# Kernel tuning notes

Hardware: AMD Instinct MI355X
Metric: run time of the kernel (lower is better)

Reference implementation:

```python
import jax, jax.numpy as jnp
import numpy as np

N_NODES = 50000
N_EDGES = 800000
D = 128
H = 128


def setup_inputs() -> dict:
    key = jax.random.key(0)
    ks = jax.random.split(key, 8)
    s = 1.0 / np.sqrt(D)
    return {
        "x": jax.random.normal(ks[0], (N_NODES, D), dtype=jnp.float32),
        "edge_index": jax.random.randint(ks[1], (2, N_EDGES), 0, N_NODES, dtype=jnp.int64),
        "W1_l": jax.random.normal(ks[2], (D, H), dtype=jnp.float32) * s,
        "b1_l": jax.random.normal(ks[3], (H,), dtype=jnp.float32) * s,
        "W1_r": jax.random.normal(ks[4], (D, H), dtype=jnp.float32) * s,
        "W2_l": jax.random.normal(ks[5], (H, H), dtype=jnp.float32) * s,
        "b2_l": jax.random.normal(ks[6], (H,), dtype=jnp.float32) * s,
        "W2_r": jax.random.normal(ks[7], (H, H), dtype=jnp.float32) * s,
    }


def _sage_conv(x, src, dst, W_l, b_l, W_r, n_nodes):
    # mean aggregation of source features at destination nodes
    agg = jax.ops.segment_sum(x[src], dst, num_segments=n_nodes)          # [N, d]
    cnt = jax.ops.segment_sum(jnp.ones((src.shape[0],), x.dtype), dst,
                              num_segments=n_nodes)                        # [N]
    mean = agg / jnp.maximum(cnt, 1.0)[:, None]
    out = mean @ W_l + b_l + x @ W_r                                       # [N, h]
    # L2 normalize (normalize=True in SAGEConv)
    norm = jnp.linalg.norm(out, axis=-1, keepdims=True)
    return out / jnp.maximum(norm, 1e-12)


def reference(x, edge_index, W1_l, b1_l, W1_r, W2_l, b2_l, W2_r):
    src, dst = edge_index[0], edge_index[1]
    n = x.shape[0]
    h = jax.nn.relu(_sage_conv(x, src, dst, W1_l, b1_l, W1_r, n))
    h = jax.nn.relu(_sage_conv(h, src, dst, W2_l, b2_l, W2_r, n))
    return h
```

## Files before the change

### kernel.cpp

```cpp
#include <hip/hip_runtime.h>

#define N_NODES 50000
#define N_EDGES 800000
#define CAP 48
#define NBUCK 391
#define NBK 98
#define EPB 8192

typedef __bf16 bf16_t;
typedef bf16_t bf16x8 __attribute__((ext_vector_type(8)));
typedef float f32x16 __attribute__((ext_vector_type(16)));

union Frag { float4 f4; bf16x8 h; };
union Pack8 { ushort u[8]; float4 f4; };

__device__ __forceinline__ ushort f2bf(float f) {
    unsigned u = __float_as_uint(f);
    return (ushort)((u + 0x7fffu + ((u >> 16) & 1u)) >> 16);
}
__device__ __forceinline__ float bf2f(unsigned bits) {
    return __uint_as_float(bits << 16);
}

__global__ __launch_bounds__(256) void prep_hist_kernel(
        const int* __restrict__ idx, int* __restrict__ flag,
        const float2* __restrict__ X, uint* __restrict__ Xb,
        const float* __restrict__ W1l, const float* __restrict__ W1r,
        const float* __restrict__ W2l, const float* __restrict__ W2r,
        ushort* __restrict__ Bp, int* __restrict__ counts) {
    __shared__ int h[NBUCK];
    __shared__ int lflag;
    int i = blockIdx.x * 256 + threadIdx.x;
    if (blockIdx.x == 0 && threadIdx.x < 64) {
        int v = idx[2 * threadIdx.x + 1];
        unsigned long long b = __ballot(v == 0);
        if (threadIdx.x == 0) *flag = (b == 0xFFFFFFFFFFFFFFFFull) ? 1 : 0;
    }
    if (i < N_NODES * 64) {
        float2 v = X[i];
        Xb[i] = ((uint)f2bf(v.y) << 16) | (uint)f2bf(v.x);
    }
    if (i < 8192) {
        int layer = i >> 12;
        int rec   = i & 4095;
        int t = rec >> 10;
        int s = (rec >> 6) & 15;
        int l = rec & 63;
        const float* Wl = layer ? W2l : W1l;
        const float* Wr = layer ? W2r : W1r;
        int n = t * 32 + (l & 31);
        int kb = s * 16 + (l >> 5) * 8;
        Pack8 o;
#pragma unroll
        for (int j = 0; j < 8; ++j) {
            int k = kb + j;
            float v = (k < 128) ? Wl[k * 128 + n] : Wr[(k - 128) * 128 + n];
            o.u[j] = f2bf(v);
        }
        *(float4*)(Bp + (size_t)i * 8) = o.f4;
    }
    if (blockIdx.x < NBK) {
        for (int t = threadIdx.x; t < NBUCK; t += 256) h[t] = 0;
        if (threadIdx.x < 64) {
            int v = idx[2 * threadIdx.x + 1];
            unsigned long long b = __ballot(v == 0);
            if (threadIdx.x == 0) lflag = (b == 0xFFFFFFFFFFFFFFFFull) ? 1 : 0;
        }
        __syncthreads();
        const int f = lflag;
        const int base = blockIdx.x * EPB;
        const int end = min(base + EPB, N_EDGES);
        for (int e = base + threadIdx.x; e < end; e += 256) {
            int dst = f ? idx[2 * N_EDGES + 2 * e] : idx[N_EDGES + e];
            atomicAdd(&h[dst >> 7], 1);
        }
        __syncthreads();
        for (int b = threadIdx.x; b < NBUCK; b += 256)
            counts[b * NBK + blockIdx.x] = h[b];
    }
}

__global__ __launch_bounds__(512) void scan_kernel(int* __restrict__ counts,
                                                   int* __restrict__ bstart) {
    __shared__ int tot[512];
    const int b = threadIdx.x;
    int s = 0;
    if (b < NBUCK)
        for (int j = 0; j < NBK; ++j) s += counts[b * NBK + j];
    tot[b] = (b < NBUCK) ? s : 0;
    __syncthreads();
    int v = tot[b];
    for (int off = 1; off < 512; off <<= 1) {
        int t = (b >= off) ? tot[b - off] : 0;
        __syncthreads();
        tot[b] += t;
        __syncthreads();
    }
    const int start = tot[b] - v;
    if (b < NBUCK) {
        int r = start;
        for (int j = 0; j < NBK; ++j) {
            int c = counts[b * NBK + j];
            counts[b * NBK + j] = r;
            r += c;
        }
        bstart[b] = start;
        if (b == NBUCK - 1) bstart[NBUCK] = start + v;
    }
}

__global__ __launch_bounds__(1024) void place_kernel(
        const int* __restrict__ idx, const int* __restrict__ flag,
        const int* __restrict__ offs, uint* __restrict__ sorted) {
    __shared__ int loc[NBUCK];
    for (int i = threadIdx.x; i < NBUCK; i += 1024)
        loc[i] = offs[i * NBK + blockIdx.x];
    __syncthreads();
    const int f = *flag;
    const int base = blockIdx.x * EPB;
    const int end = min(base + EPB, N_EDGES);
    for (int e = base + threadIdx.x; e < end; e += 1024) {
        int src, dst;
        if (f) { src = idx[2 * e]; dst = idx[2 * N_EDGES + 2 * e]; }
        else   { src = idx[e];     dst = idx[N_EDGES + e]; }
        int pos = atomicAdd(&loc[dst >> 7], 1);
        sorted[pos] = ((uint)dst << 16) | (uint)src;
    }
}

__global__ __launch_bounds__(256) void bin_kernel(
        const uint* __restrict__ sorted, const int* __restrict__ bstart,
        int* __restrict__ deg, ushort* __restrict__ esrc) {
    __shared__ int cnt[128];
    const int b = blockIdx.x;
    if (threadIdx.x < 128) cnt[threadIdx.x] = 0;
    __syncthreads();
    const int s = bstart[b], e = bstart[b + 1];
    for (int i = s + threadIdx.x; i < e; i += 256) {
        uint r = sorted[i];
        int dst = r >> 16, src = r & 0xffff;
        int pos = atomicAdd(&cnt[dst & 127], 1);
        if (pos < CAP) esrc[dst * CAP + pos] = (ushort)src;
    }
    __syncthreads();
    const int node = b * 128 + threadIdx.x;
    if (threadIdx.x < 128 && node < N_NODES) deg[node] = cnt[threadIdx.x];
}

__global__ __launch_bounds__(256) void gather_mean_kernel(
        const uint4* __restrict__ X4, const int* __restrict__ deg,
        const ushort* __restrict__ esrc, uint4* __restrict__ mean4) {
    const int node = (blockIdx.x * 256 + threadIdx.x) >> 4;
    const int l = threadIdx.x & 15;
    if (node >= N_NODES) return;
    int dg = deg[node];
    if (dg > CAP) dg = CAP;
    const ushort* es = esrc + node * CAP;

    float A0 = 0, A1 = 0, A2 = 0, A3 = 0, A4 = 0, A5 = 0, A6 = 0, A7 = 0;
    float B0 = 0, B1 = 0, B2 = 0, B3 = 0, B4 = 0, B5 = 0, B6 = 0, B7 = 0;
    int p = 0;
    for (; p + 7 < dg; p += 8) {
        ushort4 sa = *(const ushort4*)(es + p);
        ushort4 sb = *(const ushort4*)(es + p + 4);
        uint4 v0 = X4[(size_t)sa.x * 16 + l];
        uint4 v1 = X4[(size_t)sa.y * 16 + l];
        uint4 v2 = X4[(size_t)sa.z * 16 + l];
        uint4 v3 = X4[(size_t)sa.w * 16 + l];
        uint4 v4 = X4[(size_t)sb.x * 16 + l];
        uint4 v5 = X4[(size_t)sb.y * 16 + l];
        uint4 v6 = X4[(size_t)sb.z * 16 + l];
        uint4 v7 = X4[(size_t)sb.w * 16 + l];
        A0 += bf2f(v0.x & 0xffff); A1 += bf2f(v0.x >> 16);
        A2 += bf2f(v0.y & 0xffff); A3 += bf2f(v0.y >> 16);
        A4 += bf2f(v0.z & 0xffff); A5 += bf2f(v0.z >> 16);
        A6 += bf2f(v0.w & 0xffff); A7 += bf2f(v0.w >> 16);
        B0 += bf2f(v1.x & 0xffff); B1 += bf2f(v1.x >> 16);
        B2 += bf2f(v1.y & 0xffff); B3 += bf2f(v1.y >> 16);
        B4 += bf2f(v1.z & 0xffff); B5 += bf2f(v1.z >> 16);
        B6 += bf2f(v1.w & 0xffff); B7 += bf2f(v1.w >> 16);
        A0 += bf2f(v2.x & 0xffff); A1 += bf2f(v2.x >> 16);
        A2 += bf2f(v2.y & 0xffff); A3 += bf2f(v2.y >> 16);
        A4 += bf2f(v2.z & 0xffff); A5 += bf2f(v2.z >> 16);
        A6 += bf2f(v2.w & 0xffff); A7 += bf2f(v2.w >> 16);
        B0 += bf2f(v3.x & 0xffff); B1 += bf2f(v3.x >> 16);
        B2 += bf2f(v3.y & 0xffff); B3 += bf2f(v3.y >> 16);
        B4 += bf2f(v3.z & 0xffff); B5 += bf2f(v3.z >> 16);
        B6 += bf2f(v3.w & 0xffff); B7 += bf2f(v3.w >> 16);
        A0 += bf2f(v4.x & 0xffff); A1 += bf2f(v4.x >> 16);
        A2 += bf2f(v4.y & 0xffff); A3 += bf2f(v4.y >> 16);
        A4 += bf2f(v4.z & 0xffff); A5 += bf2f(v4.z >> 16);
        A6 += bf2f(v4.w & 0xffff); A7 += bf2f(v4.w >> 16);
        B0 += bf2f(v5.x & 0xffff); B1 += bf2f(v5.x >> 16);
        B2 += bf2f(v5.y & 0xffff); B3 += bf2f(v5.y >> 16);
        B4 += bf2f(v5.z & 0xffff); B5 += bf2f(v5.z >> 16);
        B6 += bf2f(v5.w & 0xffff); B7 += bf2f(v5.w >> 16);
        A0 += bf2f(v6.x & 0xffff); A1 += bf2f(v6.x >> 16);
        A2 += bf2f(v6.y & 0xffff); A3 += bf2f(v6.y >> 16);
        A4 += bf2f(v6.z & 0xffff); A5 += bf2f(v6.z >> 16);
        A6 += bf2f(v6.w & 0xffff); A7 += bf2f(v6.w >> 16);
        B0 += bf2f(v7.x & 0xffff); B1 += bf2f(v7.x >> 16);
        B2 += bf2f(v7.y & 0xffff); B3 += bf2f(v7.y >> 16);
        B4 += bf2f(v7.z & 0xffff); B5 += bf2f(v7.z >> 16);
        B6 += bf2f(v7.w & 0xffff); B7 += bf2f(v7.w >> 16);
    }
    for (; p < dg; ++p) {
        uint4 v = X4[(size_t)es[p] * 16 + l];
        A0 += bf2f(v.x & 0xffff); A1 += bf2f(v.x >> 16);
        A2 += bf2f(v.y & 0xffff); A3 += bf2f(v.y >> 16);
        A4 += bf2f(v.z & 0xffff); A5 += bf2f(v.z >> 16);
        A6 += bf2f(v.w & 0xffff); A7 += bf2f(v.w >> 16);
    }
    const float inv = 1.0f / (float)max(dg, 1);
    uint4 m;
    m.x = ((uint)f2bf((A1 + B1) * inv) << 16) | (uint)f2bf((A0 + B0) * inv);
    m.y = ((uint)f2bf((A3 + B3) * inv) << 16) | (uint)f2bf((A2 + B2) * inv);
    m.z = ((uint)f2bf((A5 + B5) * inv) << 16) | (uint)f2bf((A4 + B4) * inv);
    m.w = ((uint)f2bf((A7 + B7) * inv) << 16) | (uint)f2bf((A6 + B6) * inv);
    mean4[(size_t)node * 16 + l] = m;
}

template<bool OUT_F32>
__global__ __launch_bounds__(256) void gemm_mfma_kernel(
        const ushort* __restrict__ Amean, const ushort* Aself,
        const ushort* __restrict__ Bpack, const float* __restrict__ bias,
        void* Yout) {
    __shared__ float rs[2][64];
    const int tid = threadIdx.x;
    const int w = tid >> 6, l = tid & 63;
    const int lr = l & 31, lh = l >> 5;
    const int mrow0 = blockIdx.x * 64 + (w & 1) * 32;
    const int t0 = (w >> 1) * 2;

    f32x16 acc0, acc1;
#pragma unroll
    for (int i = 0; i < 16; ++i) { acc0[i] = 0.0f; acc1[i] = 0.0f; }

#pragma unroll
    for (int s = 0; s < 16; ++s) {
        const ushort* Ab = (s < 8) ? Amean : Aself;
        Frag a, b0, b1;
        a.f4  = *(const float4*)(Ab + (size_t)(mrow0 + lr) * 128 + (s & 7) * 16 + lh * 8);
        b0.f4 = *(const float4*)(Bpack + (size_t)(((t0) * 16 + s) * 64 + l) * 8);
        b1.f4 = *(const float4*)(Bpack + (size_t)(((t0 + 1) * 16 + s) * 64 + l) * 8);
        acc0 = __builtin_amdgcn_mfma_f32_32x32x16_bf16(a.h, b0.h, acc0, 0, 0, 0);
        acc1 = __builtin_amdgcn_mfma_f32_32x32x16_bf16(a.h, b1.h, acc1, 0, 0, 0);
    }

    const float bia0 = bias[t0 * 32 + lr];
    const float bia1 = bias[t0 * 32 + 32 + lr];
    float sq[16];
#pragma unroll
    for (int r = 0; r < 16; ++r) {
        float v0 = acc0[r] + bia0;
        float v1 = acc1[r] + bia1;
        acc0[r] = v0; acc1[r] = v1;
        float s_ = v0 * v0 + v1 * v1;
        s_ += __shfl_xor(s_, 1);
        s_ += __shfl_xor(s_, 2);
        s_ += __shfl_xor(s_, 4);
        s_ += __shfl_xor(s_, 8);
        s_ += __shfl_xor(s_, 16);
        sq[r] = s_;
    }
    if (lr == 0) {
#pragma unroll
        for (int r = 0; r < 16; ++r) {
            int rowl = (w & 1) * 32 + (r & 3) + 8 * (r >> 2) + 4 * lh;
            rs[w >> 1][rowl] = sq[r];
        }
    }
    __syncthreads();
#pragma unroll
    for (int r = 0; r < 16; ++r) {
        int rowl = (w & 1) * 32 + (r & 3) + 8 * (r >> 2) + 4 * lh;
        int grow = blockIdx.x * 64 + rowl;
        float tot = rs[0][rowl] + rs[1][rowl];
        float sc = 1.0f / fmaxf(sqrtf(tot), 1e-12f);
        if (grow < N_NODES) {
            float o0 = fmaxf(acc0[r] * sc, 0.0f);
            float o1 = fmaxf(acc1[r] * sc, 0.0f);
            if (OUT_F32) {
                float* Y = (float*)Yout;
                Y[(size_t)grow * 128 + t0 * 32 + lr]      = o0;
                Y[(size_t)grow * 128 + t0 * 32 + 32 + lr] = o1;
            } else {
                ushort* Y = (ushort*)Yout;
                Y[(size_t)grow * 128 + t0 * 32 + lr]      = f2bf(o0);
                Y[(size_t)grow * 128 + t0 * 32 + 32 + lr] = f2bf(o1);
            }
        }
    }
}

extern "C" void kernel_launch(void* const* d_in, const int* in_sizes, int n_in,
                              void* d_out, int out_size, void* d_ws, size_t ws_size,
                              hipStream_t stream) {
    const float* x    = (const float*)d_in[0];
    const int*   idx  = (const int*)d_in[1];
    const float* W1l  = (const float*)d_in[2];
    const float* b1l  = (const float*)d_in[3];
    const float* W1r  = (const float*)d_in[4];
    const float* W2l  = (const float*)d_in[5];
    const float* b2l  = (const float*)d_in[6];
    const float* W2r  = (const float*)d_in[7];
    float* out = (float*)d_out;

    int*    deg    = (int*)d_ws;
    int*    flag   = deg + N_NODES;
    ushort* esrc   = (ushort*)((int*)d_ws + 50016);
    int*    counts = (int*)d_ws + 1250016;
    int*    bstart = (int*)d_ws + 1288336;
    uint*   sorted = (uint*)((int*)d_ws + 1288736);
    uint*   meanb  = (uint*)((int*)d_ws + 2088736);
    uint*   xh     = (uint*)((int*)d_ws + 5291808);
    ushort* Bp     = (ushort*)((int*)d_ws + 8494880);

    prep_hist_kernel<<<(N_NODES * 64 + 255) / 256, 256, 0, stream>>>(
        idx, flag, (const float2*)x, xh, W1l, W1r, W2l, W2r, Bp, counts);
    scan_kernel<<<1, 512, 0, stream>>>(counts, bstart);
    place_kernel<<<NBK, 1024, 0, stream>>>(idx, flag, counts, sorted);
    bin_kernel<<<NBUCK, 256, 0, stream>>>(sorted, bstart, deg, esrc);

    const int gb = N_NODES / 16;
    const int mb = (N_NODES + 63) / 64;

    gather_mean_kernel<<<gb, 256, 0, stream>>>(
        (const uint4*)xh, deg, esrc, (uint4*)meanb);
    gemm_mfma_kernel<false><<<mb, 256, 0, stream>>>(
        (const ushort*)meanb, (const ushort*)xh, Bp, b1l, (void*)xh);
    gather_mean_kernel<<<gb, 256, 0, stream>>>(
        (const uint4*)xh, deg, esrc, (uint4*)meanb);
    gemm_mfma_kernel<true><<<mb, 256, 0, stream>>>(
        (const ushort*)meanb, (const ushort*)xh, Bp + 4096 * 8, b2l, (void*)out);
}
```

Before: 237.0 us.

## Split bf16 feature matrices into four 32-column planes for cache-local gathers

Stores node features and means as four column planes of 32 bf16 values each, instead of one row-major 128-wide matrix. The gather kernel now uses 4 lanes per node and loops over the planes in turn, and the GEMM A-loads and layer-1 output stores are re-indexed to match. The aim is to shrink the working set touched during each plane pass, so random neighbour gathers hit in L2/MALL more often. In exchange each thread does four sequential passes over its edge list, reloading the indices each time, and plane size is padded to 50048 rows.

```diff
diff --git a/kernel.cpp b/kernel.cpp
--- a/kernel.cpp
+++ b/kernel.cpp
@@ -6,6 +6,10 @@
 #define NBUCK 391
 #define NBK 98
 #define EPB 8192
+#define MROWS 50048
+#define PLANE_UI  (MROWS * 16)
+#define PLANE_U4  (MROWS * 4)
+#define PLANE_USH (MROWS * 32)
 
 typedef __bf16 bf16_t;
 typedef bf16_t bf16x8 __attribute__((ext_vector_type(8)));
@@ -38,7 +42,9 @@
     }
     if (i < N_NODES * 64) {
         float2 v = X[i];
-        Xb[i] = ((uint)f2bf(v.y) << 16) | (uint)f2bf(v.x);
+        uint packed = ((uint)f2bf(v.y) << 16) | (uint)f2bf(v.x);
+        int node = i >> 6, d2 = i & 63;
+        Xb[(size_t)(d2 >> 4) * PLANE_UI + node * 16 + (d2 & 15)] = packed;
     }
     if (i < 8192) {
         int layer = i >> 12;
@@ -150,74 +156,78 @@
 __global__ __launch_bounds__(256) void gather_mean_kernel(
         const uint4* __restrict__ X4, const int* __restrict__ deg,
         const ushort* __restrict__ esrc, uint4* __restrict__ mean4) {
-    const int node = (blockIdx.x * 256 + threadIdx.x) >> 4;
-    const int l = threadIdx.x & 15;
+    const int node = (blockIdx.x * 256 + threadIdx.x) >> 2;
+    const int l4 = threadIdx.x & 3;
     if (node >= N_NODES) return;
     int dg = deg[node];
     if (dg > CAP) dg = CAP;
     const ushort* es = esrc + node * CAP;
-
-    float A0 = 0, A1 = 0, A2 = 0, A3 = 0, A4 = 0, A5 = 0, A6 = 0, A7 = 0;
-    float B0 = 0, B1 = 0, B2 = 0, B3 = 0, B4 = 0, B5 = 0, B6 = 0, B7 = 0;
-    int p = 0;
-    for (; p + 7 < dg; p += 8) {
-        ushort4 sa = *(const ushort4*)(es + p);
-        ushort4 sb = *(const ushort4*)(es + p + 4);
-        uint4 v0 = X4[(size_t)sa.x * 16 + l];
-        uint4 v1 = X4[(size_t)sa.y * 16 + l];
-        uint4 v2 = X4[(size_t)sa.z * 16 + l];
-        uint4 v3 = X4[(size_t)sa.w * 16 + l];
-        uint4 v4 = X4[(size_t)sb.x * 16 + l];
-        uint4 v5 = X4[(size_t)sb.y * 16 + l];
-        uint4 v6 = X4[(size_t)sb.z * 16 + l];
-        uint4 v7 = X4[(size_t)sb.w * 16 + l];
-        A0 += bf2f(v0.x & 0xffff); A1 += bf2f(v0.x >> 16);
-        A2 += bf2f(v0.y & 0xffff); A3 += bf2f(v0.y >> 16);
-        A4 += bf2f(v0.z & 0xffff); A5 += bf2f(v0.z >> 16);
-        A6 += bf2f(v0.w & 0xffff); A7 += bf2f(v0.w >> 16);
-        B0 += bf2f(v1.x & 0xffff); B1 += bf2f(v1.x >> 16);
-        B2 += bf2f(v1.y & 0xffff); B3 += bf2f(v1.y >> 16);
-        B4 += bf2f(v1.z & 0xffff); B5 += bf2f(v1.z >> 16);
-        B6 += bf2f(v1.w & 0xffff); B7 += bf2f(v1.w >> 16);
-        A0 += bf2f(v2.x & 0xffff); A1 += bf2f(v2.x >> 16);
-        A2 += bf2f(v2.y & 0xffff); A3 += bf2f(v2.y >> 16);
-        A4 += bf2f(v2.z & 0xffff); A5 += bf2f(v2.z >> 16);
-        A6 += bf2f(v2.w & 0xffff); A7 += bf2f(v2.w >> 16);
-        B0 += bf2f(v3.x & 0xffff); B1 += bf2f(v3.x >> 16);
-        B2 += bf2f(v3.y & 0xffff); B3 += bf2f(v3.y >> 16);
-        B4 += bf2f(v3.z & 0xffff); B5 += bf2f(v3.z >> 16);
-        B6 += bf2f(v3.w & 0xffff); B7 += bf2f(v3.w >> 16);
-        A0 += bf2f(v4.x & 0xffff); A1 += bf2f(v4.x >> 16);
-        A2 += bf2f(v4.y & 0xffff); A3 += bf2f(v4.y >> 16);
-        A4 += bf2f(v4.z & 0xffff); A5 += bf2f(v4.z >> 16);
-        A6 += bf2f(v4.w & 0xffff); A7 += bf2f(v4.w >> 16);
-        B0 += bf2f(v5.x & 0xffff); B1 += bf2f(v5.x >> 16);
-        B2 += bf2f(v5.y & 0xffff); B3 += bf2f(v5.y >> 16);
-        B4 += bf2f(v5.z & 0xffff); B5 += bf2f(v5.z >> 16);
-        B6 += bf2f(v5.w & 0xffff); B7 += bf2f(v5.w >> 16);
-        A0 += bf2f(v6.x & 0xffff); A1 += bf2f(v6.x >> 16);
-        A2 += bf2f(v6.y & 0xffff); A3 += bf2f(v6.y >> 16);
-        A4 += bf2f(v6.z & 0xffff); A5 += bf2f(v6.z >> 16);
-        A6 += bf2f(v6.w & 0xffff); A7 += bf2f(v6.w >> 16);
-        B0 += bf2f(v7.x & 0xffff); B1 += bf2f(v7.x >> 16);
-        B2 += bf2f(v7.y & 0xffff); B3 += bf2f(v7.y >> 16);
-        B4 += bf2f(v7.z & 0xffff); B5 += bf2f(v7.z >> 16);
-        B6 += bf2f(v7.w & 0xffff); B7 += bf2f(v7.w >> 16);
-    }
-    for (; p < dg; ++p) {
-        uint4 v = X4[(size_t)es[p] * 16 + l];
-        A0 += bf2f(v.x & 0xffff); A1 += bf2f(v.x >> 16);
-        A2 += bf2f(v.y & 0xffff); A3 += bf2f(v.y >> 16);
-        A4 += bf2f(v.z & 0xffff); A5 += bf2f(v.z >> 16);
-        A6 += bf2f(v.w & 0xffff); A7 += bf2f(v.w >> 16);
-    }
     const float inv = 1.0f / (float)max(dg, 1);
-    uint4 m;
-    m.x = ((uint)f2bf((A1 + B1) * inv) << 16) | (uint)f2bf((A0 + B0) * inv);
-    m.y = ((uint)f2bf((A3 + B3) * inv) << 16) | (uint)f2bf((A2 + B2) * inv);
-    m.z = ((uint)f2bf((A5 + B5) * inv) << 16) | (uint)f2bf((A4 + B4) * inv);
-    m.w = ((uint)f2bf((A7 + B7) * inv) << 16) | (uint)f2bf((A6 + B6) * inv);
-    mean4[(size_t)node * 16 + l] = m;
+
+#pragma unroll 1
+    for (int pl = 0; pl < 4; ++pl) {
+        const uint4* __restrict__ Xp = X4 + (size_t)pl * PLANE_U4;
+        float A0 = 0, A1 = 0, A2 = 0, A3 = 0, A4 = 0, A5 = 0, A6 = 0, A7 = 0;
+        float B0 = 0, B1 = 0, B2 = 0, B3 = 0, B4 = 0, B5 = 0, B6 = 0, B7 = 0;
+        int p = 0;
+        for (; p + 7 < dg; p += 8) {
+            ushort4 sa = *(const ushort4*)(es + p);
+            ushort4 sb = *(const ushort4*)(es + p + 4);
+            uint4 v0 = Xp[(size_t)sa.x * 4 + l4];
+            uint4 v1 = Xp[(size_t)sa.y * 4 + l4];
+            uint4 v2 = Xp[(size_t)sa.z * 4 + l4];
+            uint4 v3 = Xp[(size_t)sa.w * 4 + l4];
+            uint4 v4 = Xp[(size_t)sb.x * 4 + l4];
+            uint4 v5 = Xp[(size_t)sb.y * 4 + l4];
+            uint4 v6 = Xp[(size_t)sb.z * 4 + l4];
+            uint4 v7 = Xp[(size_t)sb.w * 4 + l4];
+            A0 += bf2f(v0.x & 0xffff); A1 += bf2f(v0.x >> 16);
+            A2 += bf2f(v0.y & 0xffff); A3 += bf2f(v0.y >> 16);
+            A4 += bf2f(v0.z & 0xffff); A5 += bf2f(v0.z >> 16);
+            A6 += bf2f(v0.w & 0xffff); A7 += bf2f(v0.w >> 16);
+            B0 += bf2f(v1.x & 0xffff); B1 += bf2f(v1.x >> 16);
+            B2 += bf2f(v1.y & 0xffff); B3 += bf2f(v1.y >> 16);
+            B4 += bf2f(v1.z & 0xffff); B5 += bf2f(v1.z >> 16);
+            B6 += bf2f(v1.w & 0xffff); B7 += bf2f(v1.w >> 16);
+            A0 += bf2f(v2.x & 0xffff); A1 += bf2f(v2.x >> 16);
+            A2 += bf2f(v2.y & 0xffff); A3 += bf2f(v2.y >> 16);
+            A4 += bf2f(v2.z & 0xffff); A5 += bf2f(v2.z >> 16);
+            A6 += bf2f(v2.w & 0xffff); A7 += bf2f(v2.w >> 16);
+            B0 += bf2f(v3.x & 0xffff); B1 += bf2f(v3.x >> 16);
+            B2 += bf2f(v3.y & 0xffff); B3 += bf2f(v3.y >> 16);
+            B4 += bf2f(v3.z & 0xffff); B5 += bf2f(v3.z >> 16);
+            B6 += bf2f(v3.w & 0xffff); B7 += bf2f(v3.w >> 16);
+            A0 += bf2f(v4.x & 0xffff); A1 += bf2f(v4.x >> 16);
+            A2 += bf2f(v4.y & 0xffff); A3 += bf2f(v4.y >> 16);
+            A4 += bf2f(v4.z & 0xffff); A5 += bf2f(v4.z >> 16);
+            A6 += bf2f(v4.w & 0xffff); A7 += bf2f(v4.w >> 16);
+            B0 += bf2f(v5.x & 0xffff); B1 += bf2f(v5.x >> 16);
+            B2 += bf2f(v5.y & 0xffff); B3 += bf2f(v5.y >> 16);
+            B4 += bf2f(v5.z & 0xffff); B5 += bf2f(v5.z >> 16);
+            B6 += bf2f(v5.w & 0xffff); B7 += bf2f(v5.w >> 16);
+            A0 += bf2f(v6.x & 0xffff); A1 += bf2f(v6.x >> 16);
+            A2 += bf2f(v6.y & 0xffff); A3 += bf2f(v6.y >> 16);
+            A4 += bf2f(v6.z & 0xffff); A5 += bf2f(v6.z >> 16);
+            A6 += bf2f(v6.w & 0xffff); A7 += bf2f(v6.w >> 16);
+            B0 += bf2f(v7.x & 0xffff); B1 += bf2f(v7.x >> 16);
+            B2 += bf2f(v7.y & 0xffff); B3 += bf2f(v7.y >> 16);
+            B4 += bf2f(v7.z & 0xffff); B5 += bf2f(v7.z >> 16);
+            B6 += bf2f(v7.w & 0xffff); B7 += bf2f(v7.w >> 16);
+        }
+        for (; p < dg; ++p) {
+            uint4 v = Xp[(size_t)es[p] * 4 + l4];
+            A0 += bf2f(v.x & 0xffff); A1 += bf2f(v.x >> 16);
+            A2 += bf2f(v.y & 0xffff); A3 += bf2f(v.y >> 16);
+            A4 += bf2f(v.z & 0xffff); A5 += bf2f(v.z >> 16);
+            A6 += bf2f(v.w & 0xffff); A7 += bf2f(v.w >> 16);
+        }
+        uint4 m;
+        m.x = ((uint)f2bf((A1 + B1) * inv) << 16) | (uint)f2bf((A0 + B0) * inv);
+        m.y = ((uint)f2bf((A3 + B3) * inv) << 16) | (uint)f2bf((A2 + B2) * inv);
+        m.z = ((uint)f2bf((A5 + B5) * inv) << 16) | (uint)f2bf((A4 + B4) * inv);
+        m.w = ((uint)f2bf((A7 + B7) * inv) << 16) | (uint)f2bf((A6 + B6) * inv);
+        mean4[(size_t)pl * PLANE_U4 + node * 4 + l4] = m;
+    }
 }
 
 template<bool OUT_F32>
@@ -239,8 +249,10 @@
 #pragma unroll
     for (int s = 0; s < 16; ++s) {
         const ushort* Ab = (s < 8) ? Amean : Aself;
+        const int c = (s & 7) * 2 + lh;
         Frag a, b0, b1;
-        a.f4  = *(const float4*)(Ab + (size_t)(mrow0 + lr) * 128 + (s & 7) * 16 + lh * 8);
+        a.f4  = *(const float4*)(Ab + (size_t)(c >> 2) * PLANE_USH
+                                    + (size_t)(mrow0 + lr) * 32 + (c & 3) * 8);
         b0.f4 = *(const float4*)(Bpack + (size_t)(((t0) * 16 + s) * 64 + l) * 8);
         b1.f4 = *(const float4*)(Bpack + (size_t)(((t0 + 1) * 16 + s) * 64 + l) * 8);
         acc0 = __builtin_amdgcn_mfma_f32_32x32x16_bf16(a.h, b0.h, acc0, 0, 0, 0);
@@ -286,8 +298,8 @@
                 Y[(size_t)grow * 128 + t0 * 32 + 32 + lr] = o1;
             } else {
                 ushort* Y = (ushort*)Yout;
-                Y[(size_t)grow * 128 + t0 * 32 + lr]      = f2bf(o0);
-                Y[(size_t)grow * 128 + t0 * 32 + 32 + lr] = f2bf(o1);
+                Y[(size_t)t0       * PLANE_USH + (size_t)grow * 32 + lr] = f2bf(o0);
+                Y[(size_t)(t0 + 1) * PLANE_USH + (size_t)grow * 32 + lr] = f2bf(o1);
             }
         }
     }
@@ -322,7 +334,7 @@
     place_kernel<<<NBK, 1024, 0, stream>>>(idx, flag, counts, sorted);
     bin_kernel<<<NBUCK, 256, 0, stream>>>(sorted, bstart, deg, esrc);
 
-    const int gb = N_NODES / 16;
+    const int gb = (N_NODES + 63) / 64;
     const int mb = (N_NODES + 63) / 64;
 
     gather_mean_kernel<<<gb, 256, 0, stream>>>(
```

Result: slower. 247.1 us (+4.2%).
